# Optimization experiments

Hardware: AMD Instinct MI355X
Metric: run time of the kernel (lower is better)

The kernel has to match this reference:

```python
import jax, jax.numpy as jnp
import numpy as np

N_SRC = 50000
N_DST = 50000
E = 800000
F_IN = 128
H = 4
D = 32
NEG_SLOPE = 0.2


def setup_inputs() -> dict:
    key = jax.random.key(0)
    k1, k2, k3, k4, k5, k6, k7, k8 = jax.random.split(key, 8)
    src_feat = jax.random.normal(k1, (N_SRC, F_IN), dtype=jnp.float32)
    dst_feat = jax.random.normal(k2, (N_DST, F_IN), dtype=jnp.float32)
    edge_feat = jax.random.normal(k3, (E, F_IN), dtype=jnp.float32)
    src_idx = jax.random.randint(k4, (E,), 0, N_SRC, dtype=jnp.int32)
    dst_idx = jax.random.randint(k5, (E,), 0, N_DST, dtype=jnp.int32)
    # fc_src: in = 2*F_IN (concat op), out = H*D; fc_dst: in = F_IN, out = H*D
    g = np.sqrt(2.0)  # gain for 'relu' (xavier_normal_)
    W_src = jax.random.normal(k6, (2 * F_IN, H * D), dtype=jnp.float32) * (g * np.sqrt(2.0 / (2 * F_IN + H * D)))
    W_dst = jax.random.normal(k7, (F_IN, H * D), dtype=jnp.float32) * (g * np.sqrt(2.0 / (F_IN + H * D)))
    bias = jnp.zeros((H * D,), dtype=jnp.float32)
    return {"src_feat": src_feat, "dst_feat": dst_feat, "edge_feat": edge_feat,
            "W_src": W_src, "W_dst": W_dst, "bias": bias,
            "src_idx": src_idx, "dst_idx": dst_idx}


def reference(src_feat, dst_feat, edge_feat, W_src, W_dst, bias, src_idx, dst_idx):
    # Per-edge message: concat(src[e], edge[e]) @ W_src -> [E, H, D]
    m = jnp.concatenate([src_feat[src_idx], edge_feat], axis=1) @ W_src
    m = m.reshape(E, H, D)
    # Destination projection: [N_dst, H, D]
    nh = (dst_feat @ W_dst).reshape(N_DST, H, D)
    # e_add_v then LeakyReLU -> attention logits [E, H, D]
    scores = jax.nn.leaky_relu(m + nh[dst_idx], negative_slope=NEG_SLOPE)
    # edge_softmax: segment softmax over edges incident to each destination,
    # computed independently per (head, out_feat) channel.
    mx = jax.ops.segment_max(scores, dst_idx, num_segments=N_DST)
    ex = jnp.exp(scores - mx[dst_idx])
    denom = jax.ops.segment_sum(ex, dst_idx, num_segments=N_DST)
    attn = ex / denom[dst_idx]
    # Weighted scatter-add aggregation -> [N_dst, H, D]
    rst = jax.ops.segment_sum(m * attn, dst_idx, num_segments=N_DST)
    rst = rst + bias.reshape(1, H, D)
    return rst
```

## Files before the change

### kernel.cpp

```cpp
#include <hip/hip_runtime.h>


#define F 128
#define C 128
#define NEG 0.2f
#define NN 50000
#define EE 800000

typedef _Float16 half8 __attribute__((ext_vector_type(8)));
typedef float f32x4 __attribute__((ext_vector_type(4)));

__device__ __forceinline__ void fma4(float4& a, float s, const float4 w) {
    a.x += s * w.x; a.y += s * w.y; a.z += s * w.z; a.w += s * w.w;
}

__global__ __launch_bounds__(256) void node_proj_kernel(
    const float* __restrict__ src_feat, const float* __restrict__ dst_feat,
    const float* __restrict__ W_src, const float* __restrict__ W_dst,
    float* __restrict__ src_proj, float* __restrict__ nh)
{
    const float* in; const float* W; float* out;
    if (blockIdx.y == 0) { in = src_feat; W = W_src; out = src_proj; }
    else                 { in = dst_feat; W = W_dst; out = nh; }

    __shared__ float4 xs[8 * 32];
    const int t  = threadIdx.x;
    const int nb = blockIdx.x * 8;

    {
        int row = t >> 5, col = t & 31;
        xs[t] = ((const float4*)(in + (size_t)(nb + row) * F))[col];
    }
    __syncthreads();

    const int jq = t & 31;
    const int ng = t >> 5;
    float4 acc = make_float4(0.f, 0.f, 0.f, 0.f);
    const float4* W4 = (const float4*)W;

    #pragma unroll 4
    for (int k4 = 0; k4 < 32; ++k4) {
        float4 xv = xs[ng * 32 + k4];
        float4 w0 = W4[(4 * k4 + 0) * 32 + jq];
        float4 w1 = W4[(4 * k4 + 1) * 32 + jq];
        float4 w2 = W4[(4 * k4 + 2) * 32 + jq];
        float4 w3 = W4[(4 * k4 + 3) * 32 + jq];
        fma4(acc, xv.x, w0); fma4(acc, xv.y, w1);
        fma4(acc, xv.z, w2); fma4(acc, xv.w, w3);
    }
    ((float4*)(out + (size_t)(nb + ng) * C))[jq] = acc;
}

__global__ __launch_bounds__(256) void hist_kernel(
    const int* __restrict__ dst_idx, int* __restrict__ deg)
{
    int e = blockIdx.x * 256 + threadIdx.x;
    if (e < EE) atomicAdd(&deg[dst_idx[e]], 1);
}

__global__ __launch_bounds__(1024) void scan_kernel(
    const int* __restrict__ deg, int* __restrict__ cursor)
{
    __shared__ int ssum[1024];
    const int t = threadIdx.x;
    const int chunk = (NN + 1023) / 1024;
    int lo = t * chunk, hi = lo + chunk; if (hi > NN) hi = NN; if (lo > NN) lo = NN;
    int s = 0;
    for (int i = lo; i < hi; ++i) s += deg[i];
    ssum[t] = s;
    __syncthreads();
    for (int d = 1; d < 1024; d <<= 1) {
        int v = (t >= d) ? ssum[t - d] : 0;
        __syncthreads();
        ssum[t] += v;
        __syncthreads();
    }
    int run = ssum[t] - s;
    for (int i = lo; i < hi; ++i) { cursor[i] = run; run += deg[i]; }
}

__global__ __launch_bounds__(256) void scatter_kernel(
    const int* __restrict__ dst_idx, int* __restrict__ cursor, int* __restrict__ elist)
{
    int e = blockIdx.x * 256 + threadIdx.x;
    if (e < EE) {
        int p = atomicAdd(&cursor[dst_idx[e]], 1);
        elist[p] = e;
    }
}

__global__ __launch_bounds__(256) void prep_w_kernel(
    const float* __restrict__ W_src, _Float16* __restrict__ bfrag)
{
    int i = blockIdx.x * 256 + threadIdx.x;
    int j  = i & 7;
    int lw = (i >> 3) & 63;
    int ks = (i >> 9) & 3;
    int ct = i >> 11;
    int k  = ks * 32 + (lw >> 4) * 8 + j;
    int ch = ct * 16 + (lw & 15);
    bfrag[i] = (_Float16)W_src[(size_t)(128 + k) * 128 + ch];
}

__global__ __launch_bounds__(256) void edge_kernel(
    const float* __restrict__ edge_feat, const _Float16* __restrict__ bfrag,
    const float* __restrict__ src_proj, const float* __restrict__ nh,
    const int* __restrict__ src_idx, const int* __restrict__ dst_idx,
    const int* __restrict__ elist,
    float* __restrict__ num, float* __restrict__ den)
{
    __shared__ __align__(16) unsigned char smem[49152];
    __shared__ int sidx[64];
    __shared__ int didx[64];
    __shared__ int es[64];

    const int t  = threadIdx.x;
    const int eb = blockIdx.x * 64;

    if (t < 64) {
        int e = elist[eb + t];
        es[t] = e;
        sidx[t] = src_idx[e];
        didx[t] = dst_idx[e];
    }
    __syncthreads();

    {
        const float4* bg = (const float4*)bfrag;
        float4* bl = (float4*)(smem + 16384);
        #pragma unroll
        for (int i = 0; i < 8; ++i) bl[i * 256 + t] = bg[i * 256 + t];
    }

    #pragma unroll
    for (int i = 0; i < 4; ++i) {
        int flat = t + i * 256;
        int r = flat >> 4, c = flat & 15;
        const float4* row = (const float4*)(edge_feat + (size_t)es[r] * F);
        float4 f0 = row[2 * c], f1 = row[2 * c + 1];
        half8 h;
        h[0] = (_Float16)f0.x; h[1] = (_Float16)f0.y;
        h[2] = (_Float16)f0.z; h[3] = (_Float16)f0.w;
        h[4] = (_Float16)f1.x; h[5] = (_Float16)f1.y;
        h[6] = (_Float16)f1.z; h[7] = (_Float16)f1.w;
        *(half8*)(smem + (r << 8) + ((c ^ (r & 7)) << 4)) = h;
    }
    __syncthreads();

    const int l  = t & 63;
    const int w  = t >> 6;
    const int er = l & 15;
    const int g  = l >> 4;
    f32x4 acc[8];
    {
        f32x4 z = {0.f, 0.f, 0.f, 0.f};
        #pragma unroll
        for (int ct = 0; ct < 8; ++ct) acc[ct] = z;
    }
    #pragma unroll
    for (int ks = 0; ks < 4; ++ks) {
        half8 a = *(const half8*)(smem + ((w * 16 + er) << 8)
                                       + ((((ks << 2) + g) ^ (er & 7)) << 4));
        #pragma unroll
        for (int ct = 0; ct < 8; ++ct) {
            half8 b = *(const half8*)(smem + 16384 + ((((ct << 2) + ks) << 6) + l) * 16);
            acc[ct] = __builtin_amdgcn_mfma_f32_16x16x32_f16(a, b, acc[ct], 0, 0, 0);
        }
    }
    __syncthreads();

    float* m_lds = (float*)smem;
    #pragma unroll
    for (int ct = 0; ct < 8; ++ct) {
        #pragma unroll
        for (int rg = 0; rg < 4; ++rg) {
            m_lds[(w * 16 + g * 4 + rg) * 128 + ct * 16 + er] = acc[ct][rg];
        }
    }
    __syncthreads();

    const int jq = t & 31;
    const int eg = t >> 5;

    int cur = didx[eg * 8];
    float4 nv = ((const float4*)(nh + (size_t)cur * C))[jq];
    float4 nacc = make_float4(0.f, 0.f, 0.f, 0.f);
    float4 dacc = make_float4(0.f, 0.f, 0.f, 0.f);

    #pragma unroll
    for (int i = 0; i < 8; ++i) {
        int el = eg * 8 + i;
        int d  = didx[el];
        if (d != cur) {
            float* np = num + (size_t)cur * C + jq * 4;
            float* dp = den + (size_t)cur * C + jq * 4;
            atomicAdd(np + 0, nacc.x); atomicAdd(np + 1, nacc.y);
            atomicAdd(np + 2, nacc.z); atomicAdd(np + 3, nacc.w);
            atomicAdd(dp + 0, dacc.x); atomicAdd(dp + 1, dacc.y);
            atomicAdd(dp + 2, dacc.z); atomicAdd(dp + 3, dacc.w);
            nacc = make_float4(0.f, 0.f, 0.f, 0.f);
            dacc = make_float4(0.f, 0.f, 0.f, 0.f);
            cur = d;
            nv = ((const float4*)(nh + (size_t)d * C))[jq];
        }
        float4 mi = *(const float4*)(m_lds + el * 128 + jq * 4);
        float4 sp = ((const float4*)(src_proj + (size_t)sidx[el] * C))[jq];

        float m0 = mi.x + sp.x, m1 = mi.y + sp.y;
        float m2 = mi.z + sp.z, m3 = mi.w + sp.w;

        float s0 = m0 + nv.x, s1 = m1 + nv.y, s2 = m2 + nv.z, s3 = m3 + nv.w;
        s0 = s0 > 0.f ? s0 : NEG * s0;
        s1 = s1 > 0.f ? s1 : NEG * s1;
        s2 = s2 > 0.f ? s2 : NEG * s2;
        s3 = s3 > 0.f ? s3 : NEG * s3;

        float e0 = __expf(s0), e1 = __expf(s1), e2 = __expf(s2), e3 = __expf(s3);

        nacc.x += e0 * m0; nacc.y += e1 * m1; nacc.z += e2 * m2; nacc.w += e3 * m3;
        dacc.x += e0;      dacc.y += e1;      dacc.z += e2;      dacc.w += e3;
    }
    {
        float* np = num + (size_t)cur * C + jq * 4;
        float* dp = den + (size_t)cur * C + jq * 4;
        atomicAdd(np + 0, nacc.x); atomicAdd(np + 1, nacc.y);
        atomicAdd(np + 2, nacc.z); atomicAdd(np + 3, nacc.w);
        atomicAdd(dp + 0, dacc.x); atomicAdd(dp + 1, dacc.y);
        atomicAdd(dp + 2, dacc.z); atomicAdd(dp + 3, dacc.w);
    }
}

__global__ __launch_bounds__(256) void finalize_kernel(
    const float* __restrict__ num, const float* __restrict__ den,
    const float* __restrict__ bias, float* __restrict__ out)
{
    int i = blockIdx.x * 256 + threadIdx.x;
    float4 n = ((const float4*)num)[i];
    float4 d = ((const float4*)den)[i];
    float4 b = ((const float4*)bias)[i & 31];
    float4 r;
    r.x = (d.x != 0.f ? n.x / d.x : 0.f) + b.x;
    r.y = (d.y != 0.f ? n.y / d.y : 0.f) + b.y;
    r.z = (d.z != 0.f ? n.z / d.z : 0.f) + b.z;
    r.w = (d.w != 0.f ? n.w / d.w : 0.f) + b.w;
    ((float4*)out)[i] = r;
}

extern "C" void kernel_launch(void* const* d_in, const int* in_sizes, int n_in,
                              void* d_out, int out_size, void* d_ws, size_t ws_size,
                              hipStream_t stream) {
    const float* src_feat  = (const float*)d_in[0];
    const float* dst_feat  = (const float*)d_in[1];
    const float* edge_feat = (const float*)d_in[2];
    const float* W_src     = (const float*)d_in[3];
    const float* W_dst     = (const float*)d_in[4];
    const float* bias      = (const float*)d_in[5];
    const int*   src_idx   = (const int*)d_in[6];
    const int*   dst_idx   = (const int*)d_in[7];
    float* out = (float*)d_out;

    const size_t NODEF = (size_t)NN * C;

    float* ws       = (float*)d_ws;
    float* src_proj = ws;
    float* nh       = ws + NODEF;
    float* den      = ws + 2 * NODEF;
    int*   deg      = (int*)(ws + 3 * NODEF);
    int*   cursor   = deg + NN;
    int*   elist    = cursor + NN;
    _Float16* bfrag = (_Float16*)(elist + EE);

    float* num = out;

    hipMemsetAsync(num, 0, NODEF * sizeof(float), stream);
    hipMemsetAsync(den, 0, NODEF * sizeof(float), stream);
    hipMemsetAsync(deg, 0, NN * sizeof(int), stream);

    hist_kernel<<<(EE + 255) / 256, 256, 0, stream>>>(dst_idx, deg);
    scan_kernel<<<1, 1024, 0, stream>>>(deg, cursor);
    scatter_kernel<<<(EE + 255) / 256, 256, 0, stream>>>(dst_idx, cursor, elist);

    prep_w_kernel<<<64, 256, 0, stream>>>(W_src, bfrag);

    node_proj_kernel<<<dim3(NN / 8, 2), 256, 0, stream>>>(
        src_feat, dst_feat, W_src, W_dst, src_proj, nh);

    edge_kernel<<<EE / 64, 256, 0, stream>>>(
        edge_feat, bfrag, src_proj, nh, src_idx, dst_idx, elist, num, den);

    finalize_kernel<<<NODEF / 4 / 256, 256, 0, stream>>>(num, den, bias, out);
}
```

Baseline: 1.422 ms.

## Eliminate LDS staging in edge kernel; consume MFMA results directly in registers

The edge kernel no longer stages edge features, the weight fragments, or the MFMA output through 48KB of shared memory. Each wavefront now handles 16 edges. It loads and converts A fragments straight from global memory, reads B fragments from global memory (cached), and runs the softmax-accumulate epilogue directly on the MFMA accumulator registers, using shuffles to distribute indices. This removes the LDS traffic and barriers and frees LDS for higher occupancy. In exchange, global loads are less coalesced (scalar per-channel reads of src_proj and nh), the B fragments are re-read from L2 by every wave, and each run of edges with the same destination now issues 8 atomics per lane instead of 4-wide groups spread over 32 lanes.

```diff
diff --git a/kernel.cpp b/kernel.cpp
--- a/kernel.cpp
+++ b/kernel.cpp
@@ -109,124 +109,84 @@
     const int* __restrict__ elist,
     float* __restrict__ num, float* __restrict__ den)
 {
-    __shared__ __align__(16) unsigned char smem[49152];
-    __shared__ int sidx[64];
-    __shared__ int didx[64];
-    __shared__ int es[64];
-
-    const int t  = threadIdx.x;
-    const int eb = blockIdx.x * 64;
-
-    if (t < 64) {
-        int e = elist[eb + t];
-        es[t] = e;
-        sidx[t] = src_idx[e];
-        didx[t] = dst_idx[e];
-    }
-    __syncthreads();
-
-    {
-        const float4* bg = (const float4*)bfrag;
-        float4* bl = (float4*)(smem + 16384);
-        #pragma unroll
-        for (int i = 0; i < 8; ++i) bl[i * 256 + t] = bg[i * 256 + t];
-    }
-
-    #pragma unroll
-    for (int i = 0; i < 4; ++i) {
-        int flat = t + i * 256;
-        int r = flat >> 4, c = flat & 15;
-        const float4* row = (const float4*)(edge_feat + (size_t)es[r] * F);
-        float4 f0 = row[2 * c], f1 = row[2 * c + 1];
-        half8 h;
-        h[0] = (_Float16)f0.x; h[1] = (_Float16)f0.y;
-        h[2] = (_Float16)f0.z; h[3] = (_Float16)f0.w;
-        h[4] = (_Float16)f1.x; h[5] = (_Float16)f1.y;
-        h[6] = (_Float16)f1.z; h[7] = (_Float16)f1.w;
-        *(half8*)(smem + (r << 8) + ((c ^ (r & 7)) << 4)) = h;
-    }
-    __syncthreads();
-
-    const int l  = t & 63;
-    const int w  = t >> 6;
-    const int er = l & 15;
-    const int g  = l >> 4;
+    const int t   = threadIdx.x;
+    const int l   = t & 63;
+    const int w   = t >> 6;
+    const int ebw = (blockIdx.x * 4 + w) * 16;
+    const int er  = l & 15;
+    const int g   = l >> 4;
+
+    int e_reg = 0, s_reg = 0, d_reg = 0;
+    if (l < 16) {
+        e_reg = elist[ebw + l];
+        s_reg = src_idx[e_reg];
+        d_reg = dst_idx[e_reg];
+    }
+
+    const float4* rp = (const float4*)(edge_feat + (size_t)__shfl(e_reg, er) * F);
+    const half8*  B  = (const half8*)bfrag;
+
     f32x4 acc[8];
-    {
-        f32x4 z = {0.f, 0.f, 0.f, 0.f};
-        #pragma unroll
-        for (int ct = 0; ct < 8; ++ct) acc[ct] = z;
-    }
+    #pragma unroll
+    for (int ct = 0; ct < 8; ++ct) acc[ct] = (f32x4){0.f, 0.f, 0.f, 0.f};
+
     #pragma unroll
     for (int ks = 0; ks < 4; ++ks) {
-        half8 a = *(const half8*)(smem + ((w * 16 + er) << 8)
-                                       + ((((ks << 2) + g) ^ (er & 7)) << 4));
+        float4 f0 = rp[ks * 8 + g * 2];
+        float4 f1 = rp[ks * 8 + g * 2 + 1];
+        half8 a;
+        a[0] = (_Float16)f0.x; a[1] = (_Float16)f0.y;
+        a[2] = (_Float16)f0.z; a[3] = (_Float16)f0.w;
+        a[4] = (_Float16)f1.x; a[5] = (_Float16)f1.y;
+        a[6] = (_Float16)f1.z; a[7] = (_Float16)f1.w;
         #pragma unroll
         for (int ct = 0; ct < 8; ++ct) {
-            half8 b = *(const half8*)(smem + 16384 + ((((ct << 2) + ks) << 6) + l) * 16);
+            half8 b = B[(ct * 4 + ks) * 64 + l];
             acc[ct] = __builtin_amdgcn_mfma_f32_16x16x32_f16(a, b, acc[ct], 0, 0, 0);
         }
     }
-    __syncthreads();
-
-    float* m_lds = (float*)smem;
+
+    int cur = __shfl(d_reg, g * 4);
+    float nv[8], nacc[8], dacc[8];
     #pragma unroll
     for (int ct = 0; ct < 8; ++ct) {
+        nv[ct]   = nh[(size_t)cur * C + ct * 16 + er];
+        nacc[ct] = 0.f;
+        dacc[ct] = 0.f;
+    }
+
+    #pragma unroll
+    for (int rg = 0; rg < 4; ++rg) {
+        const int el  = g * 4 + rg;
+        const int d   = __shfl(d_reg, el);
+        const int sid = __shfl(s_reg, el);
+        if (d != cur) {
+            #pragma unroll
+            for (int ct = 0; ct < 8; ++ct) {
+                atomicAdd(num + (size_t)cur * C + ct * 16 + er, nacc[ct]);
+                atomicAdd(den + (size_t)cur * C + ct * 16 + er, dacc[ct]);
+                nacc[ct] = 0.f;
+                dacc[ct] = 0.f;
+            }
+            cur = d;
+            #pragma unroll
+            for (int ct = 0; ct < 8; ++ct) nv[ct] = nh[(size_t)cur * C + ct * 16 + er];
+        }
+        const float* sprow = src_proj + (size_t)sid * C + er;
         #pragma unroll
-        for (int rg = 0; rg < 4; ++rg) {
-            m_lds[(w * 16 + g * 4 + rg) * 128 + ct * 16 + er] = acc[ct][rg];
+        for (int ct = 0; ct < 8; ++ct) {
+            float m = acc[ct][rg] + sprow[ct * 16];
+            float s = m + nv[ct];
+            s = s > 0.f ? s : NEG * s;
+            float ex = __expf(s);
+            nacc[ct] += ex * m;
+            dacc[ct] += ex;
         }
     }
-    __syncthreads();
-
-    const int jq = t & 31;
-    const int eg = t >> 5;
-
-    int cur = didx[eg * 8];
-    float4 nv = ((const float4*)(nh + (size_t)cur * C))[jq];
-    float4 nacc = make_float4(0.f, 0.f, 0.f, 0.f);
-    float4 dacc = make_float4(0.f, 0.f, 0.f, 0.f);
-
-    #pragma unroll
-    for (int i = 0; i < 8; ++i) {
-        int el = eg * 8 + i;
-        int d  = didx[el];
-        if (d != cur) {
-            float* np = num + (size_t)cur * C + jq * 4;
-            float* dp = den + (size_t)cur * C + jq * 4;
-            atomicAdd(np + 0, nacc.x); atomicAdd(np + 1, nacc.y);
-            atomicAdd(np + 2, nacc.z); atomicAdd(np + 3, nacc.w);
-            atomicAdd(dp + 0, dacc.x); atomicAdd(dp + 1, dacc.y);
-            atomicAdd(dp + 2, dacc.z); atomicAdd(dp + 3, dacc.w);
-            nacc = make_float4(0.f, 0.f, 0.f, 0.f);
-            dacc = make_float4(0.f, 0.f, 0.f, 0.f);
-            cur = d;
-            nv = ((const float4*)(nh + (size_t)d * C))[jq];
-        }
-        float4 mi = *(const float4*)(m_lds + el * 128 + jq * 4);
-        float4 sp = ((const float4*)(src_proj + (size_t)sidx[el] * C))[jq];
-
-        float m0 = mi.x + sp.x, m1 = mi.y + sp.y;
-        float m2 = mi.z + sp.z, m3 = mi.w + sp.w;
-
-        float s0 = m0 + nv.x, s1 = m1 + nv.y, s2 = m2 + nv.z, s3 = m3 + nv.w;
-        s0 = s0 > 0.f ? s0 : NEG * s0;
-        s1 = s1 > 0.f ? s1 : NEG * s1;
-        s2 = s2 > 0.f ? s2 : NEG * s2;
-        s3 = s3 > 0.f ? s3 : NEG * s3;
-
-        float e0 = __expf(s0), e1 = __expf(s1), e2 = __expf(s2), e3 = __expf(s3);
-
-        nacc.x += e0 * m0; nacc.y += e1 * m1; nacc.z += e2 * m2; nacc.w += e3 * m3;
-        dacc.x += e0;      dacc.y += e1;      dacc.z += e2;      dacc.w += e3;
-    }
-    {
-        float* np = num + (size_t)cur * C + jq * 4;
-        float* dp = den + (size_t)cur * C + jq * 4;
-        atomicAdd(np + 0, nacc.x); atomicAdd(np + 1, nacc.y);
-        atomicAdd(np + 2, nacc.z); atomicAdd(np + 3, nacc.w);
-        atomicAdd(dp + 0, dacc.x); atomicAdd(dp + 1, dacc.y);
-        atomicAdd(dp + 2, dacc.z); atomicAdd(dp + 3, dacc.w);
+    #pragma unroll
+    for (int ct = 0; ct < 8; ++ct) {
+        atomicAdd(num + (size_t)cur * C + ct * 16 + er, nacc[ct]);
+        atomicAdd(den + (size_t)cur * C + ct * 16 + er, dacc[ct]);
     }
 }
 
```

Measured after the change: 1.448 ms. Within noise of the previous version (+1.9%).
